# Kernel tuning notes

Measured on AMD Instinct MI355X. Metric: run time of the kernel, lower is better.

The kernel has to match this reference:

```python
import jax, jax.numpy as jnp
import numpy as np

B, T, D_IN, H, K, C = 8, 2048, 512, 384, 8192, 8
N_BLOCKS = 6
EPS = 1e-5


def conv1d(x, w, b, pad, groups=1):
    # x: [B, Cin, T], w: [Cout, Cin//groups, k]
    y = jax.lax.conv_general_dilated(
        x, w, window_strides=(1,), padding=[(pad, pad)],
        dimension_numbers=("NCH", "OIH", "NCH"), feature_group_count=groups)
    return y + b[None, :, None]


def layernorm(x, g, b):
    # normalize over last axis
    m = jnp.mean(x, axis=-1, keepdims=True)
    v = jnp.mean(jnp.square(x - m), axis=-1, keepdims=True)
    return (x - m) * jax.lax.rsqrt(v + EPS) * g + b


def setup_inputs() -> dict:
    key = jax.random.key(0)
    ks = iter(jax.random.split(key, 32))
    s = 0.02
    inp = {
        "x": jax.random.normal(next(ks), (B, T, D_IN), dtype=jnp.float32),
        "enc_w": jax.random.normal(next(ks), (H, D_IN, 7)) * s,
        "enc_b": jnp.zeros((H,)),
        "enc_ln_g": jnp.ones((H,)),
        "enc_ln_b": jnp.zeros((H,)),
        "blk_dw_w": jax.random.normal(next(ks), (N_BLOCKS, H, 1, 7)) * s,
        "blk_dw_b": jnp.zeros((N_BLOCKS, H)),
        "blk_ln_g": jnp.ones((N_BLOCKS, H)),
        "blk_ln_b": jnp.zeros((N_BLOCKS, H)),
        "blk_w1": jax.random.normal(next(ks), (N_BLOCKS, 4 * H, H)) * s,
        "blk_b1": jnp.zeros((N_BLOCKS, 4 * H)),
        "blk_w2": jax.random.normal(next(ks), (N_BLOCKS, H, 4 * H)) * s,
        "blk_b2": jnp.zeros((N_BLOCKS, H)),
        "out_w": jax.random.normal(next(ks), (C, H, 1)) * s,
        "out_b": jnp.zeros((C,)),
        "embeddings": jax.random.normal(next(ks), (K, C)),
    }
    return inp


def encode(x, enc_w, enc_b, enc_ln_g, enc_ln_b, blk_dw_w, blk_dw_b,
           blk_ln_g, blk_ln_b, blk_w1, blk_b1, blk_w2, blk_b2, out_w, out_b):
    h = x.transpose(0, 2, 1)                       # [B, D_IN, T]
    h = conv1d(h, enc_w, enc_b, pad=3)             # [B, H, T]
    h = layernorm(h.transpose(0, 2, 1), enc_ln_g, enc_ln_b).transpose(0, 2, 1)
    for i in range(N_BLOCKS):
        res = h
        h = conv1d(h, blk_dw_w[i], blk_dw_b[i], pad=3, groups=H)  # depthwise
        ht = h.transpose(0, 2, 1)                  # [B, T, H]
        ht = layernorm(ht, blk_ln_g[i], blk_ln_b[i])
        ht = jnp.einsum("bth,fh->btf", ht, blk_w1[i]) + blk_b1[i]
        ht = jax.nn.gelu(ht, approximate=False)    # torch GELU is exact erf
        ht = jnp.einsum("btf,hf->bth", ht, blk_w2[i]) + blk_b2[i]
        h = ht.transpose(0, 2, 1) + res
    z = conv1d(h, out_w, out_b, pad=0)             # [B, C, T]
    return z.transpose(0, 2, 1)                    # [B, T, C]


def reference(x, enc_w, enc_b, enc_ln_g, enc_ln_b, blk_dw_w, blk_dw_b,
              blk_ln_g, blk_ln_b, blk_w1, blk_b1, blk_w2, blk_b2,
              out_w, out_b, embeddings):
    z = encode(x, enc_w, enc_b, enc_ln_g, enc_ln_b, blk_dw_w, blk_dw_b,
               blk_ln_g, blk_ln_b, blk_w1, blk_b1, blk_w2, blk_b2, out_w, out_b)
    flat = z.reshape(-1, C)                        # [B*T, C]
    # squared euclidean distances: same argmin as torch.cdist
    d2 = (jnp.sum(flat * flat, axis=1, keepdims=True)
          - 2.0 * flat @ embeddings.T
          + jnp.sum(embeddings * embeddings, axis=1))  # [B*T, K]
    indices = jnp.argmin(d2, axis=1)               # [B*T], int
    return indices
```

## Files before the change

kernel.cpp:

```cpp
#include <hip/hip_runtime.h>
#include <math.h>

#define T_   2048
#define DIN  512
#define H_   384
#define H4_  1536
#define BT_  16384

typedef _Float16 half_t;
typedef _Float16 f16x8 __attribute__((ext_vector_type(8)));
typedef float f32x4 __attribute__((ext_vector_type(4)));

#define LO_SCALE 2048.0f
#define LO_INV   4.8828125e-4f

__device__ __forceinline__ void lds_barrier() {
    asm volatile("s_waitcnt lgkmcnt(0)\n\ts_barrier" ::: "memory");
}

__device__ __forceinline__ void split2(float v, half_t* hi, half_t* lo) {
    half_t h = (half_t)v;
    *hi = h;
    *lo = (half_t)((v - (float)h) * LO_SCALE);
}

__global__ void k_split(const float* __restrict__ in, half_t* __restrict__ hi,
                        half_t* __restrict__ lo, long n) {
    long i = (long)blockIdx.x * 256 + threadIdx.x;
    if (i >= n) return;
    split2(in[i], hi + i, lo + i);
}

__global__ void k_split_encw(const float* __restrict__ in, half_t* __restrict__ hi,
                             half_t* __restrict__ lo) {
    int idx = blockIdx.x * 256 + threadIdx.x;
    if (idx >= H_ * 3584) return;
    int n = idx / 3584;
    int r = idx % 3584;
    int tap = r >> 9, i = r & 511;
    split2(in[n * 3584 + i * 7 + tap], hi + idx, lo + idx);
}

__global__ void k_ln(const float* __restrict__ in, float* __restrict__ out,
                     const float* __restrict__ g, const float* __restrict__ b) {
    int row = blockIdx.x;
    int lane = threadIdx.x;
    const float* ir = in + (long)row * H_;
    float v[6];
    float s = 0.f;
#pragma unroll
    for (int j = 0; j < 6; ++j) { v[j] = ir[lane + (j << 6)]; s += v[j]; }
#pragma unroll
    for (int o = 32; o > 0; o >>= 1) s += __shfl_down(s, o, 64);
    s = __shfl(s, 0, 64);
    float mean = s * (1.f / 384.f);
    float q = 0.f;
#pragma unroll
    for (int j = 0; j < 6; ++j) { float d = v[j] - mean; q += d * d; }
#pragma unroll
    for (int o = 32; o > 0; o >>= 1) q += __shfl_down(q, o, 64);
    q = __shfl(q, 0, 64);
    float rstd = rsqrtf(q * (1.f / 384.f) + 1e-5f);
    float* orow = out + (long)row * H_;
#pragma unroll
    for (int j = 0; j < 6; ++j) {
        int c = lane + (j << 6);
        orow[c] = (v[j] - mean) * rstd * g[c] + b[c];
    }
}

__global__ void k_dwconv_ln(const float* __restrict__ h, half_t* __restrict__ oh,
                            half_t* __restrict__ ol,
                            const float* __restrict__ w, const float* __restrict__ wb,
                            const float* __restrict__ g, const float* __restrict__ gb) {
    int row = blockIdx.x;
    int b = row >> 11;
    int t = row & 2047;
    int lane = threadIdx.x;
    const float* hb = h + ((long)b * T_) * H_;
    float v[6];
    float s = 0.f;
#pragma unroll
    for (int j = 0; j < 6; ++j) {
        int c = lane + (j << 6);
        float acc = wb[c];
        const float* wc = w + c * 7;
#pragma unroll
        for (int k = 0; k < 7; ++k) {
            int tt = t + k - 3;
            if ((unsigned)tt < (unsigned)T_)
                acc = fmaf(hb[(long)tt * H_ + c], wc[k], acc);
        }
        v[j] = acc;
        s += acc;
    }
#pragma unroll
    for (int o = 32; o > 0; o >>= 1) s += __shfl_down(s, o, 64);
    s = __shfl(s, 0, 64);
    float mean = s * (1.f / 384.f);
    float q = 0.f;
#pragma unroll
    for (int j = 0; j < 6; ++j) { float d = v[j] - mean; q += d * d; }
#pragma unroll
    for (int o = 32; o > 0; o >>= 1) q += __shfl_down(q, o, 64);
    q = __shfl(q, 0, 64);
    float rstd = rsqrtf(q * (1.f / 384.f) + 1e-5f);
    long ro = (long)row * H_;
#pragma unroll
    for (int j = 0; j < 6; ++j) {
        int c = lane + (j << 6);
        float val = (v[j] - mean) * rstd * g[c] + gb[c];
        split2(val, oh + ro + c, ol + ro + c);
    }
}

template <int MODE>
__global__ __launch_bounds__(256) void k_mgemm(
    const half_t* __restrict__ Ah, const half_t* __restrict__ Al,
    const half_t* __restrict__ Bh, const half_t* __restrict__ Bl,
    const float* __restrict__ bias, const float* __restrict__ res,
    float* __restrict__ Cf, half_t* __restrict__ Ch, half_t* __restrict__ Cl,
    int N, int K) {
    __shared__ __align__(16) half_t smem[30720];
    const int tid = threadIdx.x;
    const int lane = tid & 63, wid = tid >> 6;
    const int wm = (wid >> 1) << 6, wn = (wid & 1) << 5;
    const int quad = lane >> 4, l16 = lane & 15;
    const int m0 = blockIdx.y << 7, n0 = blockIdx.x << 6;
    const int ar = tid >> 2;
    const int ak = (tid & 3) << 3;
    const int br = tid >> 2, bk = (tid & 3) << 3;

    long aoff0 = 0, aoff1 = 0;
    int tt0 = 0, tt1 = 0, bq = 0;
    if (MODE == 0) {
        bq = m0 >> 11;
        tt0 = (m0 & 2047) + ar - 3;
        tt1 = tt0 + 64;
    } else {
        aoff0 = (long)(m0 + ar) * K + ak;
        aoff1 = aoff0 + (long)64 * K;
    }
    const long boff = (long)(n0 + br) * K + bk;

    float4 pa0h, pa0l, pa1h, pa1l, pbh, pbl;
    auto loadregs = [&](int k0) {
        if (MODE == 0) {
            int kk = k0 + ak;
            int tap = kk >> 9, ii = kk & 511;
            int ta = tt0 + tap, tb = tt1 + tap;
            pa0h = pa0l = pa1h = pa1l = make_float4(0.f, 0.f, 0.f, 0.f);
            if ((unsigned)ta < 2048u) {
                long o = ((long)bq * 2048 + ta) * 512 + ii;
                pa0h = *(const float4*)(Ah + o);
                pa0l = *(const float4*)(Al + o);
            }
            if ((unsigned)tb < 2048u) {
                long o = ((long)bq * 2048 + tb) * 512 + ii;
                pa1h = *(const float4*)(Ah + o);
                pa1l = *(const float4*)(Al + o);
            }
        } else {
            pa0h = *(const float4*)(Ah + aoff0 + k0);
            pa0l = *(const float4*)(Al + aoff0 + k0);
            pa1h = *(const float4*)(Ah + aoff1 + k0);
            pa1l = *(const float4*)(Al + aoff1 + k0);
        }
        pbh = *(const float4*)(Bh + boff + k0);
        pbl = *(const float4*)(Bl + boff + k0);
    };
    const int aw = ar * 40 + ak;
    const int bw = br * 40 + bk;
    auto storebuf = [&](int buf) {
        *(float4*)&smem[buf * 5120 + aw] = pa0h;
        *(float4*)&smem[buf * 5120 + aw + 2560] = pa1h;
        *(float4*)&smem[10240 + buf * 5120 + aw] = pa0l;
        *(float4*)&smem[10240 + buf * 5120 + aw + 2560] = pa1l;
        *(float4*)&smem[20480 + buf * 2560 + bw] = pbh;
        *(float4*)&smem[25600 + buf * 2560 + bw] = pbl;
    };

    f32x4 acc1[4][2] = {};
    f32x4 acc2[4][2] = {};

    loadregs(0);
    storebuf(0);
    const int nIter = K >> 5;
    int cur = 0;
    for (int it = 0; it < nIter; ++it) {
        if (it + 1 < nIter) loadregs((it + 1) << 5);
        lds_barrier();
        const int af = cur * 5120 + (wm + l16) * 40 + quad * 8;
        const int bf = cur * 2560 + (wn + l16) * 40 + quad * 8;
        f16x8 fah[4], fal[4], fgh[2], fgl[2];
#pragma unroll
        for (int f = 0; f < 4; ++f) {
            fah[f] = *(const f16x8*)&smem[af + f * 640];
            fal[f] = *(const f16x8*)&smem[10240 + af + f * 640];
        }
#pragma unroll
        for (int g = 0; g < 2; ++g) {
            fgh[g] = *(const f16x8*)&smem[20480 + bf + g * 640];
            fgl[g] = *(const f16x8*)&smem[25600 + bf + g * 640];
        }
#pragma unroll
        for (int f = 0; f < 4; ++f)
#pragma unroll
            for (int g = 0; g < 2; ++g)
                acc2[f][g] = __builtin_amdgcn_mfma_f32_16x16x32_f16(fah[f], fgl[g], acc2[f][g], 0, 0, 0);
#pragma unroll
        for (int f = 0; f < 4; ++f)
#pragma unroll
            for (int g = 0; g < 2; ++g)
                acc2[f][g] = __builtin_amdgcn_mfma_f32_16x16x32_f16(fal[f], fgh[g], acc2[f][g], 0, 0, 0);
#pragma unroll
        for (int f = 0; f < 4; ++f)
#pragma unroll
            for (int g = 0; g < 2; ++g)
                acc1[f][g] = __builtin_amdgcn_mfma_f32_16x16x32_f16(fah[f], fgh[g], acc1[f][g], 0, 0, 0);
        if (it + 1 < nIter) storebuf(cur ^ 1);
        cur ^= 1;
    }

    float bv[2];
    bv[0] = bias[n0 + wn + l16];
    bv[1] = bias[n0 + wn + 16 + l16];

    if (MODE == 1) {
        __syncthreads();
#pragma unroll
        for (int f = 0; f < 4; ++f)
#pragma unroll
            for (int g = 0; g < 2; ++g)
#pragma unroll
                for (int r = 0; r < 4; ++r) {
                    int rm = wm + f * 16 + quad * 4 + r;
                    int cn = wn + g * 16 + l16;
                    float v = acc1[f][g][r] + acc2[f][g][r] * LO_INV + bv[g];
                    v = 0.5f * v * (1.0f + erff(v * 0.70710678118654752f));
                    half_t hh = (half_t)v;
                    smem[rm * 72 + cn] = hh;
                    smem[9216 + rm * 72 + cn] = (half_t)((v - (float)hh) * LO_SCALE);
                }
        __syncthreads();
#pragma unroll
        for (int s = 0; s < 4; ++s) {
            int idx = tid + (s << 8);
            int row = idx >> 3, c8 = (idx & 7) << 3;
            long go = (long)(m0 + row) * N + n0 + c8;
            *(float4*)(Ch + go) = *(const float4*)&smem[row * 72 + c8];
            *(float4*)(Cl + go) = *(const float4*)&smem[9216 + row * 72 + c8];
        }
    } else {
#pragma unroll
        for (int f = 0; f < 4; ++f)
#pragma unroll
            for (int g = 0; g < 2; ++g)
#pragma unroll
                for (int r = 0; r < 4; ++r) {
                    long row = m0 + wm + f * 16 + quad * 4 + r;
                    int col = n0 + wn + g * 16 + l16;
                    float v = acc1[f][g][r] + acc2[f][g][r] * LO_INV + bv[g];
                    long o = row * N + col;
                    if (MODE == 2) v += res[o];
                    Cf[o] = v;
                }
    }
}

__global__ __launch_bounds__(256) void k_outconv_argmin(
    const float* __restrict__ h, const float* __restrict__ ow,
    const float* __restrict__ ob, const float* __restrict__ emb,
    int* __restrict__ outIdx) {
    __shared__ float hs[16][H_ + 1];
    __shared__ float zs[16][8];
    __shared__ float es[16 * 516];
    __shared__ float rb[16][16];
    __shared__ int ri[16][16];
    const int tid = threadIdx.x;
    const int row0 = blockIdx.x << 4;

    for (int i = tid; i < 16 * (H_ / 4); i += 256) {
        int r = i / 96;
        int c4 = (i % 96) << 2;
        float4 v = *(const float4*)&h[((long)(row0 + r)) * H_ + c4];
        hs[r][c4] = v.x; hs[r][c4 + 1] = v.y; hs[r][c4 + 2] = v.z; hs[r][c4 + 3] = v.w;
    }
    __syncthreads();

    if (tid < 128) {
        int r = tid & 15, c = tid >> 4;
        float acc = ob[c];
        const float* wc = ow + c * H_;
        for (int j = 0; j < H_; ++j) acc = fmaf(hs[r][j], wc[j], acc);
        zs[r][c] = acc;
    }
    __syncthreads();

    const int r = tid & 15;
    const int sl = tid >> 4;
    float z0 = zs[r][0], z1 = zs[r][1], z2 = zs[r][2], z3 = zs[r][3];
    float z4 = zs[r][4], z5 = zs[r][5], z6 = zs[r][6], z7 = zs[r][7];
    float best = 3.4e38f;
    int bi = 0;

    for (int ch = 0; ch < 8; ++ch) {
        __syncthreads();
        for (int i = tid; i < 2048; i += 256) {
            int e = i >> 1;
            int half = (i & 1) << 2;
            float4 src = *(const float4*)&emb[(((long)(ch << 10)) + e) * 8 + half];
            *(float4*)&es[(e >> 6) * 516 + ((e & 63) << 3) + half] = src;
        }
        __syncthreads();
        const float* ep = es + sl * 516;
        int gbase = (ch << 10) + (sl << 6);
#pragma unroll 4
        for (int j = 0; j < 64; ++j) {
            float4 e0 = *(const float4*)(ep + (j << 3));
            float4 e1 = *(const float4*)(ep + (j << 3) + 4);
            float t, d;
            t = e0.x - z0; d = t * t;
            t = e0.y - z1; d = fmaf(t, t, d);
            t = e0.z - z2; d = fmaf(t, t, d);
            t = e0.w - z3; d = fmaf(t, t, d);
            t = e1.x - z4; d = fmaf(t, t, d);
            t = e1.y - z5; d = fmaf(t, t, d);
            t = e1.z - z6; d = fmaf(t, t, d);
            t = e1.w - z7; d = fmaf(t, t, d);
            if (d < best) { best = d; bi = gbase + j; }
        }
    }
    rb[r][sl] = best;
    ri[r][sl] = bi;
    __syncthreads();
    if (sl == 0) {
        float bb = rb[r][0];
        int bbi = ri[r][0];
#pragma unroll
        for (int s2 = 1; s2 < 16; ++s2) {
            float v = rb[r][s2];
            int i2 = ri[r][s2];
            if (v < bb || (v == bb && i2 < bbi)) { bb = v; bbi = i2; }
        }
        outIdx[row0 + r] = bbi;
    }
}

extern "C" void kernel_launch(void* const* d_in, const int* in_sizes, int n_in,
                              void* d_out, int out_size, void* d_ws, size_t ws_size,
                              hipStream_t stream) {
    const float* x        = (const float*)d_in[0];
    const float* enc_w    = (const float*)d_in[1];
    const float* enc_b    = (const float*)d_in[2];
    const float* enc_ln_g = (const float*)d_in[3];
    const float* enc_ln_b = (const float*)d_in[4];
    const float* blk_dw_w = (const float*)d_in[5];
    const float* blk_dw_b = (const float*)d_in[6];
    const float* blk_ln_g = (const float*)d_in[7];
    const float* blk_ln_b = (const float*)d_in[8];
    const float* blk_w1   = (const float*)d_in[9];
    const float* blk_b1   = (const float*)d_in[10];
    const float* blk_w2   = (const float*)d_in[11];
    const float* blk_b2   = (const float*)d_in[12];
    const float* out_w    = (const float*)d_in[13];
    const float* out_b    = (const float*)d_in[14];
    const float* emb      = (const float*)d_in[15];
    int* out = (int*)d_out;

    char* base = (char*)d_ws;
    float*  h    = (float*)base;
    half_t* tmph = (half_t*)(base + 25165824);
    half_t* tmpl = (half_t*)(base + 37748736);
    half_t* ht4h = (half_t*)(base + 50331648);
    half_t* ht4l = (half_t*)(base + 100663296);
    half_t* ench = (half_t*)(base + 150994944);
    half_t* encl = (half_t*)(base + 153747456);
    half_t* w1h  = (half_t*)(base + 156499968);
    half_t* w1l  = (half_t*)(base + 163577856);
    half_t* w2h  = (half_t*)(base + 170655744);
    half_t* w2l  = (half_t*)(base + 177733632);
    half_t* xh = ht4h;
    half_t* xl = (half_t*)(base + 50331648 + 16777216);

    k_split<<<(8388608 + 255) / 256, 256, 0, stream>>>(x, xh, xl, 8388608L);
    k_split<<<(3538944 + 255) / 256, 256, 0, stream>>>(blk_w1, w1h, w1l, 3538944L);
    k_split<<<(3538944 + 255) / 256, 256, 0, stream>>>(blk_w2, w2h, w2l, 3538944L);
    k_split_encw<<<(H_ * 3584 + 255) / 256, 256, 0, stream>>>(enc_w, ench, encl);

    k_mgemm<0><<<dim3(6, 128), 256, 0, stream>>>(xh, xl, ench, encl, enc_b,
                                                 nullptr, h, nullptr, nullptr,
                                                 H_, 3584);
    k_ln<<<BT_, 64, 0, stream>>>(h, h, enc_ln_g, enc_ln_b);

    for (int i = 0; i < 6; ++i) {
        k_dwconv_ln<<<BT_, 64, 0, stream>>>(h, tmph, tmpl, blk_dw_w + i * H_ * 7,
                                            blk_dw_b + i * H_, blk_ln_g + i * H_,
                                            blk_ln_b + i * H_);
        k_mgemm<1><<<dim3(24, 128), 256, 0, stream>>>(
            tmph, tmpl, w1h + (long)i * 589824, w1l + (long)i * 589824,
            blk_b1 + i * H4_, nullptr, nullptr, ht4h, ht4l, H4_, H_);
        k_mgemm<2><<<dim3(6, 128), 256, 0, stream>>>(
            ht4h, ht4l, w2h + (long)i * 589824, w2l + (long)i * 589824,
            blk_b2 + i * H_, h, h, nullptr, nullptr, H_, H4_);
    }

    k_outconv_argmin<<<BT_ / 16, 256, 0, stream>>>(h, out_w, out_b, emb, out);
}
```

Baseline: 1.987 ms.

## Enlarge GEMM tile to 128x128 using 32x32x16 MFMA and swap grid order

The split-fp16 GEMM kernel moves from a 128x64 block tile with 16x16x32 MFMAs to a 128x128 tile where each wave computes 64x64 using 32x32x16 MFMAs. Shared memory grows to hold the larger B tile, and the epilogue layout is rewritten for the 32x32 accumulator mapping. The grid is transposed so that blockIdx.x walks M, which changes which blocks run at the same time and share B tiles in cache. The aim is higher arithmetic intensity per LDS load and fewer blocks, at the cost of more registers and LDS and fewer blocks for small N (3 column tiles).

```diff
diff --git a/kernel.cpp b/kernel.cpp
--- a/kernel.cpp
+++ b/kernel.cpp
@@ -9,7 +9,7 @@
 
 typedef _Float16 half_t;
 typedef _Float16 f16x8 __attribute__((ext_vector_type(8)));
-typedef float f32x4 __attribute__((ext_vector_type(4)));
+typedef float f32x16 __attribute__((ext_vector_type(16)));
 
 #define LO_SCALE 2048.0f
 #define LO_INV   4.8828125e-4f
@@ -114,6 +114,10 @@
     }
 }
 
+__device__ __forceinline__ float gelu_exact(float x) {
+    return 0.5f * x * (1.0f + erff(x * 0.70710678118654752f));
+}
+
 template <int MODE>
 __global__ __launch_bounds__(256) void k_mgemm(
     const half_t* __restrict__ Ah, const half_t* __restrict__ Al,
@@ -121,67 +125,61 @@
     const float* __restrict__ bias, const float* __restrict__ res,
     float* __restrict__ Cf, half_t* __restrict__ Ch, half_t* __restrict__ Cl,
     int N, int K) {
-    __shared__ __align__(16) half_t smem[30720];
+    __shared__ __align__(16) half_t smem[40960];
     const int tid = threadIdx.x;
     const int lane = tid & 63, wid = tid >> 6;
-    const int wm = (wid >> 1) << 6, wn = (wid & 1) << 5;
-    const int quad = lane >> 4, l16 = lane & 15;
-    const int m0 = blockIdx.y << 7, n0 = blockIdx.x << 6;
-    const int ar = tid >> 2;
-    const int ak = (tid & 3) << 3;
-    const int br = tid >> 2, bk = (tid & 3) << 3;
-
-    long aoff0 = 0, aoff1 = 0;
-    int tt0 = 0, tt1 = 0, bq = 0;
+    const int wm = (wid >> 1) << 6, wn = (wid & 1) << 6;
+    const int l32 = lane & 31, sh = lane >> 5;
+    const int m0 = blockIdx.x << 7, n0 = blockIdx.y << 7;
+    const int sr = tid >> 1;
+    const int sk = (tid & 1) << 4;
+
+    long abase = 0;
+    int tbase = 0, bq = 0;
     if (MODE == 0) {
         bq = m0 >> 11;
-        tt0 = (m0 & 2047) + ar - 3;
-        tt1 = tt0 + 64;
+        tbase = (m0 & 2047) + sr - 3;
     } else {
-        aoff0 = (long)(m0 + ar) * K + ak;
-        aoff1 = aoff0 + (long)64 * K;
-    }
-    const long boff = (long)(n0 + br) * K + bk;
-
-    float4 pa0h, pa0l, pa1h, pa1l, pbh, pbl;
+        abase = (long)(m0 + sr) * K + sk;
+    }
+    const long bbase = (long)(n0 + sr) * K + sk;
+
+    float4 pAh[2], pAl[2], pBh[2], pBl[2];
     auto loadregs = [&](int k0) {
         if (MODE == 0) {
-            int kk = k0 + ak;
+            int kk = k0 + sk;
             int tap = kk >> 9, ii = kk & 511;
-            int ta = tt0 + tap, tb = tt1 + tap;
-            pa0h = pa0l = pa1h = pa1l = make_float4(0.f, 0.f, 0.f, 0.f);
-            if ((unsigned)ta < 2048u) {
-                long o = ((long)bq * 2048 + ta) * 512 + ii;
-                pa0h = *(const float4*)(Ah + o);
-                pa0l = *(const float4*)(Al + o);
-            }
-            if ((unsigned)tb < 2048u) {
-                long o = ((long)bq * 2048 + tb) * 512 + ii;
-                pa1h = *(const float4*)(Ah + o);
-                pa1l = *(const float4*)(Al + o);
+            int tt = tbase + tap;
+            pAh[0] = pAh[1] = pAl[0] = pAl[1] = make_float4(0.f, 0.f, 0.f, 0.f);
+            if ((unsigned)tt < 2048u) {
+                long o = ((long)bq * 2048 + tt) * 512 + ii;
+                pAh[0] = *(const float4*)(Ah + o);
+                pAh[1] = *(const float4*)(Ah + o + 8);
+                pAl[0] = *(const float4*)(Al + o);
+                pAl[1] = *(const float4*)(Al + o + 8);
             }
         } else {
-            pa0h = *(const float4*)(Ah + aoff0 + k0);
-            pa0l = *(const float4*)(Al + aoff0 + k0);
-            pa1h = *(const float4*)(Ah + aoff1 + k0);
-            pa1l = *(const float4*)(Al + aoff1 + k0);
-        }
-        pbh = *(const float4*)(Bh + boff + k0);
-        pbl = *(const float4*)(Bl + boff + k0);
+            pAh[0] = *(const float4*)(Ah + abase + k0);
+            pAh[1] = *(const float4*)(Ah + abase + k0 + 8);
+            pAl[0] = *(const float4*)(Al + abase + k0);
+            pAl[1] = *(const float4*)(Al + abase + k0 + 8);
+        }
+        pBh[0] = *(const float4*)(Bh + bbase + k0);
+        pBh[1] = *(const float4*)(Bh + bbase + k0 + 8);
+        pBl[0] = *(const float4*)(Bl + bbase + k0);
+        pBl[1] = *(const float4*)(Bl + bbase + k0 + 8);
     };
-    const int aw = ar * 40 + ak;
-    const int bw = br * 40 + bk;
     auto storebuf = [&](int buf) {
-        *(float4*)&smem[buf * 5120 + aw] = pa0h;
-        *(float4*)&smem[buf * 5120 + aw + 2560] = pa1h;
-        *(float4*)&smem[10240 + buf * 5120 + aw] = pa0l;
-        *(float4*)&smem[10240 + buf * 5120 + aw + 2560] = pa1l;
-        *(float4*)&smem[20480 + buf * 2560 + bw] = pbh;
-        *(float4*)&smem[25600 + buf * 2560 + bw] = pbl;
+        int a0 = ((buf * 2 + 0) * 128 + sr) * 40 + sk;
+        int a1 = ((buf * 2 + 1) * 128 + sr) * 40 + sk;
+        *(float4*)&smem[a0] = pAh[0];      *(float4*)&smem[a0 + 8] = pAh[1];
+        *(float4*)&smem[a1] = pAl[0];      *(float4*)&smem[a1 + 8] = pAl[1];
+        *(float4*)&smem[20480 + a0] = pBh[0]; *(float4*)&smem[20480 + a0 + 8] = pBh[1];
+        *(float4*)&smem[20480 + a1] = pBl[0]; *(float4*)&smem[20480 + a1 + 8] = pBl[1];
     };
 
-    f32x4 acc1[4][2] = {};
-    f32x4 acc2[4][2] = {};
+    f32x16 acc1[2][2] = {};
+    f32x16 acc2[2][2] = {};
 
     loadregs(0);
     storebuf(0);
@@ -190,77 +188,74 @@
     for (int it = 0; it < nIter; ++it) {
         if (it + 1 < nIter) loadregs((it + 1) << 5);
         lds_barrier();
-        const int af = cur * 5120 + (wm + l16) * 40 + quad * 8;
-        const int bf = cur * 2560 + (wn + l16) * 40 + quad * 8;
-        f16x8 fah[4], fal[4], fgh[2], fgl[2];
-#pragma unroll
-        for (int f = 0; f < 4; ++f) {
-            fah[f] = *(const f16x8*)&smem[af + f * 640];
-            fal[f] = *(const f16x8*)&smem[10240 + af + f * 640];
-        }
-#pragma unroll
-        for (int g = 0; g < 2; ++g) {
-            fgh[g] = *(const f16x8*)&smem[20480 + bf + g * 640];
-            fgl[g] = *(const f16x8*)&smem[25600 + bf + g * 640];
-        }
-#pragma unroll
-        for (int f = 0; f < 4; ++f)
-#pragma unroll
-            for (int g = 0; g < 2; ++g)
-                acc2[f][g] = __builtin_amdgcn_mfma_f32_16x16x32_f16(fah[f], fgl[g], acc2[f][g], 0, 0, 0);
-#pragma unroll
-        for (int f = 0; f < 4; ++f)
-#pragma unroll
-            for (int g = 0; g < 2; ++g)
-                acc2[f][g] = __builtin_amdgcn_mfma_f32_16x16x32_f16(fal[f], fgh[g], acc2[f][g], 0, 0, 0);
-#pragma unroll
-        for (int f = 0; f < 4; ++f)
-#pragma unroll
-            for (int g = 0; g < 2; ++g)
-                acc1[f][g] = __builtin_amdgcn_mfma_f32_16x16x32_f16(fah[f], fgh[g], acc1[f][g], 0, 0, 0);
+#pragma unroll
+        for (int kc = 0; kc < 2; ++kc) {
+            const int ko = kc * 16 + sh * 8;
+            f16x8 fah[2], fal[2], fbh[2], fbl[2];
+#pragma unroll
+            for (int mi = 0; mi < 2; ++mi) {
+                int r = wm + mi * 32 + l32;
+                fah[mi] = *(const f16x8*)&smem[((cur * 2 + 0) * 128 + r) * 40 + ko];
+                fal[mi] = *(const f16x8*)&smem[((cur * 2 + 1) * 128 + r) * 40 + ko];
+            }
+#pragma unroll
+            for (int ni = 0; ni < 2; ++ni) {
+                int r = wn + ni * 32 + l32;
+                fbh[ni] = *(const f16x8*)&smem[20480 + ((cur * 2 + 0) * 128 + r) * 40 + ko];
+                fbl[ni] = *(const f16x8*)&smem[20480 + ((cur * 2 + 1) * 128 + r) * 40 + ko];
+            }
+#pragma unroll
+            for (int mi = 0; mi < 2; ++mi)
+#pragma unroll
+                for (int ni = 0; ni < 2; ++ni) {
+                    acc2[mi][ni] = __builtin_amdgcn_mfma_f32_32x32x16_f16(fah[mi], fbl[ni], acc2[mi][ni], 0, 0, 0);
+                    acc2[mi][ni] = __builtin_amdgcn_mfma_f32_32x32x16_f16(fal[mi], fbh[ni], acc2[mi][ni], 0, 0, 0);
+                    acc1[mi][ni] = __builtin_amdgcn_mfma_f32_32x32x16_f16(fah[mi], fbh[ni], acc1[mi][ni], 0, 0, 0);
+                }
+        }
         if (it + 1 < nIter) storebuf(cur ^ 1);
         cur ^= 1;
     }
 
     float bv[2];
-    bv[0] = bias[n0 + wn + l16];
-    bv[1] = bias[n0 + wn + 16 + l16];
+#pragma unroll
+    for (int ni = 0; ni < 2; ++ni) bv[ni] = bias[n0 + wn + ni * 32 + l32];
 
     if (MODE == 1) {
         __syncthreads();
 #pragma unroll
-        for (int f = 0; f < 4; ++f)
-#pragma unroll
-            for (int g = 0; g < 2; ++g)
-#pragma unroll
-                for (int r = 0; r < 4; ++r) {
-                    int rm = wm + f * 16 + quad * 4 + r;
-                    int cn = wn + g * 16 + l16;
-                    float v = acc1[f][g][r] + acc2[f][g][r] * LO_INV + bv[g];
-                    v = 0.5f * v * (1.0f + erff(v * 0.70710678118654752f));
+        for (int mi = 0; mi < 2; ++mi)
+#pragma unroll
+            for (int ni = 0; ni < 2; ++ni)
+#pragma unroll
+                for (int i = 0; i < 16; ++i) {
+                    int lr = wm + mi * 32 + (i & 3) + 8 * (i >> 2) + 4 * sh;
+                    int lc = wn + ni * 32 + l32;
+                    float v = acc1[mi][ni][i] + acc2[mi][ni][i] * LO_INV + bv[ni];
+                    v = gelu_exact(v);
                     half_t hh = (half_t)v;
-                    smem[rm * 72 + cn] = hh;
-                    smem[9216 + rm * 72 + cn] = (half_t)((v - (float)hh) * LO_SCALE);
+                    smem[lr * 136 + lc] = hh;
+                    smem[17408 + lr * 136 + lc] = (half_t)((v - (float)hh) * LO_SCALE);
                 }
         __syncthreads();
 #pragma unroll
-        for (int s = 0; s < 4; ++s) {
+        for (int s = 0; s < 8; ++s) {
             int idx = tid + (s << 8);
-            int row = idx >> 3, c8 = (idx & 7) << 3;
+            int row = idx >> 4, c8 = (idx & 15) << 3;
             long go = (long)(m0 + row) * N + n0 + c8;
-            *(float4*)(Ch + go) = *(const float4*)&smem[row * 72 + c8];
-            *(float4*)(Cl + go) = *(const float4*)&smem[9216 + row * 72 + c8];
+            *(float4*)(Ch + go) = *(const float4*)&smem[row * 136 + c8];
+            *(float4*)(Cl + go) = *(const float4*)&smem[17408 + row * 136 + c8];
         }
     } else {
 #pragma unroll
-        for (int f = 0; f < 4; ++f)
-#pragma unroll
-            for (int g = 0; g < 2; ++g)
-#pragma unroll
-                for (int r = 0; r < 4; ++r) {
-                    long row = m0 + wm + f * 16 + quad * 4 + r;
-                    int col = n0 + wn + g * 16 + l16;
-                    float v = acc1[f][g][r] + acc2[f][g][r] * LO_INV + bv[g];
+        for (int mi = 0; mi < 2; ++mi)
+#pragma unroll
+            for (int ni = 0; ni < 2; ++ni)
+#pragma unroll
+                for (int i = 0; i < 16; ++i) {
+                    long row = m0 + wm + mi * 32 + (i & 3) + 8 * (i >> 2) + 4 * sh;
+                    int col = n0 + wn + ni * 32 + l32;
+                    float v = acc1[mi][ni][i] + acc2[mi][ni][i] * LO_INV + bv[ni];
                     long o = row * N + col;
                     if (MODE == 2) v += res[o];
                     Cf[o] = v;
@@ -388,7 +383,7 @@
     k_split<<<(3538944 + 255) / 256, 256, 0, stream>>>(blk_w2, w2h, w2l, 3538944L);
     k_split_encw<<<(H_ * 3584 + 255) / 256, 256, 0, stream>>>(enc_w, ench, encl);
 
-    k_mgemm<0><<<dim3(6, 128), 256, 0, stream>>>(xh, xl, ench, encl, enc_b,
+    k_mgemm<0><<<dim3(128, 3), 256, 0, stream>>>(xh, xl, ench, encl, enc_b,
                                                  nullptr, h, nullptr, nullptr,
                                                  H_, 3584);
     k_ln<<<BT_, 64, 0, stream>>>(h, h, enc_ln_g, enc_ln_b);
@@ -397,10 +392,10 @@
         k_dwconv_ln<<<BT_, 64, 0, stream>>>(h, tmph, tmpl, blk_dw_w + i * H_ * 7,
                                             blk_dw_b + i * H_, blk_ln_g + i * H_,
                                             blk_ln_b + i * H_);
-        k_mgemm<1><<<dim3(24, 128), 256, 0, stream>>>(
+        k_mgemm<1><<<dim3(128, 12), 256, 0, stream>>>(
             tmph, tmpl, w1h + (long)i * 589824, w1l + (long)i * 589824,
             blk_b1 + i * H4_, nullptr, nullptr, ht4h, ht4l, H4_, H_);
-        k_mgemm<2><<<dim3(6, 128), 256, 0, stream>>>(
+        k_mgemm<2><<<dim3(128, 3), 256, 0, stream>>>(
             ht4h, ht4l, w2h + (long)i * 589824, w2l + (long)i * 589824,
             blk_b2 + i * H_, h, h, nullptr, nullptr, H_, H4_);
     }
```

Measured after the change: 3.715 ms. 1.87x slower.
